# Performance work log

Hardware: AMD Instinct MI355X
Metric: run time of the kernel (lower is better)

The kernel has to match this reference:

```python
import jax, jax.numpy as jnp
import numpy as np

D_MODEL = 1024
N_HEADS = 16
FEAT_DIM = 16   # q/k head dim before feature-map expansion
V_DIM = 64      # v head dim = d_model / n_heads
EPS = 1e-12


def taylor_exp(x):
    """2nd-order Taylor approx feature map of exp(q^T k / sqrt(d)).
    x: (b, h, l, d) -> (b, h, l, 1 + d + d^2)
    f(x) = [1, x / d^{1/4}, vec(x x^T) / (sqrt(2) * sqrt(d))]
    """
    d = x.shape[-1]
    rd = jnp.sqrt(jnp.float32(d))          # sqrt(d)
    rrd = jnp.sqrt(rd)                     # d^{1/4}
    r2 = jnp.sqrt(jnp.float32(2.0))
    x2 = (x[..., :, None] * x[..., None, :]).reshape(*x.shape[:-1], d * d) / r2
    ones = jnp.ones(x.shape[:-1] + (1,), dtype=x.dtype)
    return jnp.concatenate([ones, x / rrd, x2 / rd], axis=-1)


def setup_inputs() -> dict:
    key = jax.random.key(0)
    k0, k1, k2, k3, k4 = jax.random.split(key, 5)
    b, l = 2, 2048
    scale = 1.0 / np.sqrt(D_MODEL)
    return {
        "hidden_states": jax.random.normal(k0, (b, l, D_MODEL), dtype=jnp.float32),
        "Wq": jax.random.normal(k1, (D_MODEL, N_HEADS * FEAT_DIM), dtype=jnp.float32) * scale,
        "Wk": jax.random.normal(k2, (D_MODEL, N_HEADS * FEAT_DIM), dtype=jnp.float32) * scale,
        "Wv": jax.random.normal(k3, (D_MODEL, N_HEADS * V_DIM), dtype=jnp.float32) * scale,
        "Wo": jax.random.normal(k4, (N_HEADS * V_DIM, D_MODEL), dtype=jnp.float32) * scale,
    }


def reference(hidden_states, Wq, Wk, Wv, Wo):
    b, l, _ = hidden_states.shape
    # projections -> (b, h, l, d)
    q = (hidden_states @ Wq).reshape(b, l, N_HEADS, FEAT_DIM).transpose(0, 2, 1, 3)
    k = (hidden_states @ Wk).reshape(b, l, N_HEADS, FEAT_DIM).transpose(0, 2, 1, 3)
    v = (hidden_states @ Wv).reshape(b, l, N_HEADS, V_DIM).transpose(0, 2, 1, 3)

    qf = taylor_exp(q)  # (b, h, l, 273)
    kf = taylor_exp(k)

    # causal linear attention (naive parallel form used by the torch module)
    A = jnp.einsum('bhnf,bhmf->bhnm', qf, kf)
    A = jnp.tril(A)
    y = jnp.einsum('bhnm,bhme->bhne', A, v)
    # denominator: q_f . cumsum(k_f)
    z = 1.0 / (jnp.einsum('bhlf,bhlf->bhl', qf, jnp.cumsum(kf, axis=2)) + EPS)
    y = y * z[..., None]

    out = y.transpose(0, 2, 1, 3).reshape(b, l, N_HEADS * V_DIM) @ Wo
    return out
```

## Files before the change

### kernel.cpp

```cpp
#include <hip/hip_runtime.h>
#include <hip/hip_bf16.h>

#define BATCH 2
#define LSEQ 2048
#define DMODEL 1024
#define NH 16
#define DQK 16
#define DV 64
#define FDIM 273
#define CHUNK 128
#define NCH (LSEQ / CHUNK)
#define ROWS (BATCH * LSEQ)
#define NBH (BATCH * NH)
#define NBC (NBH * NCH)
#define QKVW 1536
#define C2 0.17677669529663687f

typedef short bf16x8 __attribute__((ext_vector_type(8)));
typedef float f32x4 __attribute__((ext_vector_type(4)));

__device__ __forceinline__ unsigned short f2bf(float f) {
  __hip_bfloat16 h = __float2bfloat16(f);
  unsigned short u; __builtin_memcpy(&u, &h, 2); return u;
}
__device__ __forceinline__ float bf2f(unsigned short u) {
  unsigned int v = (unsigned int)u << 16; float f; __builtin_memcpy(&f, &v, 4); return f;
}

__device__ __forceinline__ void storeC(float* C, size_t off, float v) { C[off] = v; }
__device__ __forceinline__ void storeC(unsigned short* C, size_t off, float v) {
  C[off] = f2bf(v);
}

__global__ __launch_bounds__(256) void prep(
    const float* __restrict__ hs,
    const float* __restrict__ Wq, const float* __restrict__ Wk,
    const float* __restrict__ Wv, const float* __restrict__ Wo,
    unsigned short* __restrict__ hsb,
    unsigned short* __restrict__ wqt, unsigned short* __restrict__ wkt,
    unsigned short* __restrict__ wvt, unsigned short* __restrict__ wot) {
  __shared__ float t[32][33];
  if (blockIdx.z == 4) {
    int bid = blockIdx.y * 32 + blockIdx.x;
    const float4* in4 = (const float4*)hs;
#pragma unroll
    for (int k = 0; k < 4; k++) {
      int i = bid * 1024 + k * 256 + threadIdx.x;
      float4 v = in4[i];
      ushort4 o = {f2bf(v.x), f2bf(v.y), f2bf(v.z), f2bf(v.w)};
      ((ushort4*)hsb)[i] = o;
    }
    return;
  }
  const float* W; unsigned short* Wt; int N;
  switch (blockIdx.z) {
    case 0: W = Wq; Wt = wqt; N = 256; break;
    case 1: W = Wk; Wt = wkt; N = 256; break;
    case 2: W = Wv; Wt = wvt; N = 1024; break;
    default: W = Wo; Wt = wot; N = 1024; break;
  }
  const int nb = blockIdx.x * 32;
  if (nb >= N) return;
  const int kb = blockIdx.y * 32;
  const int tx = threadIdx.x & 31, ty4 = (threadIdx.x >> 5) * 4;
#pragma unroll
  for (int r = 0; r < 4; r++)
    t[ty4 + r][tx] = W[(size_t)(kb + ty4 + r) * N + nb + tx];
  __syncthreads();
#pragma unroll
  for (int r = 0; r < 4; r++)
    Wt[(size_t)(nb + ty4 + r) * DMODEL + kb + tx] = f2bf(t[tx][ty4 + r]);
}

template <typename CT>
__global__ __launch_bounds__(256) void gemm_pipe(
    const unsigned short* __restrict__ A, const unsigned short* __restrict__ Bt,
    CT* __restrict__ C, int M, int N, int K) {
  __shared__ unsigned short Sbuf[4 * 8192];
  const int tid = threadIdx.x;
  const int nwg = gridDim.x * gridDim.y;
  const int bid0 = blockIdx.y * gridDim.x + blockIdx.x;
  const int bid = (bid0 & 7) * (nwg >> 3) + (bid0 >> 3);
  const int bm = (bid / gridDim.x) * 128, bn = (bid % gridDim.x) * 128;
  const int lane = tid & 63;
  const int w = tid >> 6;
  const int qr = (w >> 1) * 64, qc = (w & 1) * 64;
  const int nk = K >> 5;
  f32x4 acc[4][4] = {};

  const unsigned short* gbase[4];
  int loff[4];
#pragma unroll
  for (int j = 0; j < 4; ++j) {
    int c = j * 256 + tid;
    int isB = c >> 9;
    int cc = c & 511;
    int row = ((cc >> 6) << 4) + (cc & 15);
    int kh = (cc >> 4) & 3;
    gbase[j] = (isB ? Bt + (size_t)(bn + row) * K : A + (size_t)(bm + row) * K) + kh * 8;
    loff[j] = isB * 4096 + cc * 8;
  }
  auto stage = [&](int t) {
    unsigned short* Sb = Sbuf + (size_t)(t & 3) * 8192;
#pragma unroll
    for (int j = 0; j < 4; ++j)
      __builtin_amdgcn_global_load_lds(
          (const __attribute__((address_space(1))) unsigned int*)(const void*)(gbase[j] + (t << 5)),
          (__attribute__((address_space(3))) unsigned int*)(Sb + loff[j]), 16, 0, 0);
  };

  stage(0); stage(1); stage(2);

  for (int tt = 0; tt < nk; tt += 2) {
    if (tt + 3 < nk) {
      stage(tt + 3);
      asm volatile("s_waitcnt vmcnt(8)" ::: "memory");
    } else {
      asm volatile("s_waitcnt vmcnt(0)" ::: "memory");
    }
    __builtin_amdgcn_s_barrier();
    asm volatile("" ::: "memory");

    const unsigned short* Ab0 = Sbuf + (size_t)(tt & 3) * 8192;
    const unsigned short* Ab1 = Sbuf + (size_t)((tt + 1) & 3) * 8192;
    bf16x8 a0[4], b0[4], a1[4], b1[4];
#pragma unroll
    for (int i = 0; i < 4; ++i) {
      a0[i] = *(const bf16x8*)(Ab0 + ((qr >> 4) + i) * 512 + lane * 8);
      b0[i] = *(const bf16x8*)(Ab0 + 4096 + ((qc >> 4) + i) * 512 + lane * 8);
      a1[i] = *(const bf16x8*)(Ab1 + ((qr >> 4) + i) * 512 + lane * 8);
      b1[i] = *(const bf16x8*)(Ab1 + 4096 + ((qc >> 4) + i) * 512 + lane * 8);
    }
    __builtin_amdgcn_s_setprio(1);
#pragma unroll
    for (int i = 0; i < 4; ++i)
#pragma unroll
      for (int jj = 0; jj < 4; ++jj)
        acc[i][jj] = __builtin_amdgcn_mfma_f32_16x16x32_bf16(a0[i], b0[jj], acc[i][jj], 0, 0, 0);
#pragma unroll
    for (int i = 0; i < 4; ++i)
#pragma unroll
      for (int jj = 0; jj < 4; ++jj)
        acc[i][jj] = __builtin_amdgcn_mfma_f32_16x16x32_bf16(a1[i], b1[jj], acc[i][jj], 0, 0, 0);
    __builtin_amdgcn_s_setprio(0);

    asm volatile("" ::: "memory");
    __builtin_amdgcn_s_barrier();
    asm volatile("" ::: "memory");
    if (tt + 4 < nk) stage(tt + 4);
  }

  const int cn = lane & 15, r0 = (lane >> 4) * 4;
#pragma unroll
  for (int i = 0; i < 4; ++i)
#pragma unroll
    for (int jj = 0; jj < 4; ++jj) {
      size_t base = (size_t)(bm + qr + i * 16 + r0) * N + bn + qc + jj * 16 + cn;
#pragma unroll
      for (int r = 0; r < 4; ++r) storeC(C, base + (size_t)r * N, acc[i][jj][r]);
    }
}

__device__ __forceinline__ void stage_Vp(const unsigned short* __restrict__ qkvb,
                                         int row0, int h, int tid, short* Vp) {
#pragma unroll
  for (int it = 0; it < 4; it++) {
    int t = it * 256 + tid;
    int j = t >> 3, e0 = (t & 7) * 8;
    bf16x8 v8 = *(const bf16x8*)(qkvb + (size_t)(row0 + j) * QKVW + 512 + h * 64 + e0);
    int jg = j >> 3, jj = j & 7;
#pragma unroll
    for (int u = 0; u < 8; u++) {
      int e = e0 + u;
      Vp[((e >> 4) * 4 + (jg >> 2)) * 512 + ((jg & 3) * 16 + (e & 15)) * 8 + jj] =
          v8[u];
    }
  }
  {
    int n = tid & 15, jgrp = tid >> 4;
    bf16x8 v8;
#pragma unroll
    for (int u = 0; u < 8; u++) v8[u] = (n == 0) ? (short)0x3F80 : (short)0;
    *(bf16x8*)(Vp + (16 + (jgrp >> 2)) * 512 + ((jgrp & 3) * 16 + n) * 8) = v8;
  }
}

__global__ __launch_bounds__(256) void chunk_sums_mfma(
    const unsigned short* __restrict__ qkvb, unsigned short* __restrict__ Sfrag) {
  const int c = blockIdx.x, bh = blockIdx.y;
  const int b = bh >> 4, h = bh & 15;
  const int tid = threadIdx.x;
  const int lane = tid & 63, w = tid >> 6;
  const int row0 = b * LSEQ + c * CHUNK;

  __shared__ float ksT[16 * 132];
  __shared__ short SH[56 * 512];
  short* Vp = SH;
  short* Kf0 = SH + 20 * 512;
  short* Kf1 = SH + 38 * 512;

  {
    int i = tid >> 1, d0 = (tid & 1) * 8;
    bf16x8 k8 = *(const bf16x8*)(qkvb + (size_t)(row0 + i) * QKVW + 256 + h * 16 + d0);
#pragma unroll
    for (int j = 0; j < 8; j++) ksT[(d0 + j) * 132 + i] = bf2f((unsigned short)k8[j]);
  }
  stage_Vp(qkvb, row0, h, tid, Vp);
  __syncthreads();

  auto gen = [&](int kt, short* dst) {
    for (int o = tid; o < 1152; o += 256) {
      int mt = o >> 6, w6 = o & 63;
      int kh = w6 >> 4, m = w6 & 15;
      int f = mt * 16 + m;
      int i0 = kt * 32 + kh * 8;
      bf16x8 v8;
      if (f == 0) {
#pragma unroll
        for (int j = 0; j < 8; j++) v8[j] = (short)0x3F80;
      } else if (f < 17) {
        const float* ka = &ksT[(f - 1) * 132 + i0];
        float4 a0 = *(const float4*)ka, a1 = *(const float4*)(ka + 4);
        v8[0] = (short)f2bf(0.5f * a0.x); v8[1] = (short)f2bf(0.5f * a0.y);
        v8[2] = (short)f2bf(0.5f * a0.z); v8[3] = (short)f2bf(0.5f * a0.w);
        v8[4] = (short)f2bf(0.5f * a1.x); v8[5] = (short)f2bf(0.5f * a1.y);
        v8[6] = (short)f2bf(0.5f * a1.z); v8[7] = (short)f2bf(0.5f * a1.w);
      } else if (f < FDIM) {
        int ix = f - 17;
        const float* ka = &ksT[(ix >> 4) * 132 + i0];
        const float* kb2 = &ksT[(ix & 15) * 132 + i0];
        float4 a0 = *(const float4*)ka, a1 = *(const float4*)(ka + 4);
        float4 b0 = *(const float4*)kb2, b1 = *(const float4*)(kb2 + 4);
        v8[0] = (short)f2bf(C2 * a0.x * b0.x); v8[1] = (short)f2bf(C2 * a0.y * b0.y);
        v8[2] = (short)f2bf(C2 * a0.z * b0.z); v8[3] = (short)f2bf(C2 * a0.w * b0.w);
        v8[4] = (short)f2bf(C2 * a1.x * b1.x); v8[5] = (short)f2bf(C2 * a1.y * b1.y);
        v8[6] = (short)f2bf(C2 * a1.z * b1.z); v8[7] = (short)f2bf(C2 * a1.w * b1.w);
      } else {
#pragma unroll
        for (int j = 0; j < 8; j++) v8[j] = 0;
      }
      *(bf16x8*)(dst + mt * 512 + (kh * 16 + m) * 8) = v8;
    }
  };

  gen(0, Kf0);
  __syncthreads();

  f32x4 acc[5][5] = {};
  const int nmt = (w < 2) ? 5 : 4;
  for (int kt = 0; kt < 4; kt++) {
    short* cur = (kt & 1) ? Kf1 : Kf0;
    if (kt < 3) gen(kt + 1, (kt & 1) ? Kf0 : Kf1);
    bf16x8 bv[5];
#pragma unroll
    for (int nt = 0; nt < 5; nt++)
      bv[nt] = *(const bf16x8*)(Vp + (nt * 4 + kt) * 512 + lane * 8);
#pragma unroll
    for (int t2 = 0; t2 < 5; t2++) {
      if (t2 < nmt) {
        int mt = w + t2 * 4;
        bf16x8 av = *(const bf16x8*)(cur + mt * 512 + lane * 8);
#pragma unroll
        for (int nt = 0; nt < 5; nt++)
          acc[t2][nt] = __builtin_amdgcn_mfma_f32_16x16x32_bf16(av, bv[nt], acc[t2][nt], 0, 0, 0);
      }
    }
    __syncthreads();
  }

  const int cl = lane & 15, r0q = (lane >> 4) * 4;
#pragma unroll
  for (int t2 = 0; t2 < 5; t2++) {
    if (t2 < nmt) {
      int mt = w + t2 * 4;
#pragma unroll
      for (int reg = 0; reg < 4; reg++) {
        int f = mt * 16 + r0q + reg;
#pragma unroll
        for (int nt = 0; nt < 5; nt++) {
          int e = nt * 16 + cl;
          SH[((f >> 5) * 5 + nt) * 512 + (((f >> 3) & 3) * 16 + (e & 15)) * 8 + (f & 7)] =
              (short)f2bf(acc[t2][nt][reg]);
        }
      }
    }
  }
  __syncthreads();
  unsigned short* dst = Sfrag + ((size_t)bh * NCH + c) * 45 * 512;
  for (int o = tid; o < 2880; o += 256)
    *(bf16x8*)(dst + o * 8) = *(const bf16x8*)(SH + o * 8);
}

__global__ __launch_bounds__(64) void prefix_scan_frag(
    const unsigned short* __restrict__ Sfrag, unsigned short* __restrict__ PG) {
  const int kt5 = blockIdx.x, bh = blockIdx.y;
  const int lane = threadIdx.x;
  float run[8] = {0.f, 0.f, 0.f, 0.f, 0.f, 0.f, 0.f, 0.f};
  const size_t base = ((size_t)bh * NCH * 45 + kt5) * 512 + lane * 8;
#pragma unroll
  for (int cc = 0; cc < NCH; cc++) {
    size_t a = base + (size_t)cc * 45 * 512;
    bf16x8 s8 = *(const bf16x8*)(Sfrag + a);
    bf16x8 o8;
#pragma unroll
    for (int j = 0; j < 8; j++) {
      o8[j] = (short)f2bf(run[j]);
      run[j] += bf2f((unsigned short)s8[j]);
    }
    *(bf16x8*)(PG + a) = o8;
  }
}

__global__ __launch_bounds__(256) void attn_mfma(
    const unsigned short* __restrict__ qkvb, const unsigned short* __restrict__ PG,
    unsigned short* __restrict__ ybuf) {
  const int c = blockIdx.x, bh = blockIdx.y;
  const int b = bh >> 4, h = bh & 15;
  const int tid = threadIdx.x;
  const int lane = tid & 63, w = tid >> 6;
  const int row0 = b * LSEQ + c * CHUNK;

  __shared__ short U[36864];
  __shared__ float denL[128];
  unsigned short* Uu = (unsigned short*)U;

  const int qrow = (w >> 1) * 64 + lane;
  const int shalf = w & 1;
  bf16x8 qa = *(const bf16x8*)(qkvb + (size_t)(row0 + qrow) * QKVW + h * 16);
  bf16x8 qb = *(const bf16x8*)(qkvb + (size_t)(row0 + qrow) * QKVW + h * 16 + 8);

  for (int t = tid; t < 1024; t += 256) {
    int isK = t >> 9;
    int tt = t & 511;
    int i = tt >> 2, kh = tt & 3;
    bf16x8 v8 = {0, 0, 0, 0, 0, 0, 0, 0};
    if (kh < 2)
      v8 = *(const bf16x8*)(qkvb + (size_t)(row0 + i) * QKVW + isK * 256 + h * 16 + kh * 8);
    *(bf16x8*)(U + isK * 4096 + (i >> 4) * 512 + (kh * 16 + (i & 15)) * 8) = v8;
  }
  __syncthreads();

  {
    bf16x8 aq[2];
#pragma unroll
    for (int mi = 0; mi < 2; mi++)
      aq[mi] = *(const bf16x8*)(U + (w * 2 + mi) * 512 + lane * 8);
    f32x4 S[2][8] = {};
#pragma unroll
    for (int nt = 0; nt < 8; nt++) {
      bf16x8 bk = *(const bf16x8*)(U + 4096 + nt * 512 + lane * 8);
#pragma unroll
      for (int mi = 0; mi < 2; mi++)
        S[mi][nt] = __builtin_amdgcn_mfma_f32_16x16x32_bf16(aq[mi], bk, S[mi][nt], 0, 0, 0);
    }
    const int cl = lane & 15, r0q = (lane >> 4) * 4;
#pragma unroll
    for (int mi = 0; mi < 2; mi++)
#pragma unroll
      for (int nt = 0; nt < 8; nt++)
#pragma unroll
        for (int reg = 0; reg < 4; reg++) {
          int i = (w * 2 + mi) * 16 + r0q + reg;
          int j = nt * 16 + cl;
          float s = S[mi][nt][reg];
          float aij = (j <= i) ? fmaf(s, fmaf(s, 0.03125f, 0.25f), 1.0f) : 0.0f;
          U[8192 + ((i >> 4) * 4 + (j >> 5)) * 512 +
            (((j >> 3) & 3) * 16 + (i & 15)) * 8 + (j & 7)] = (short)f2bf(aij);
        }
  }
  stage_Vp(qkvb, row0, h, tid, U + 24576);
  __syncthreads();

  f32x4 Y[2][5] = {};
#pragma unroll
  for (int kc = 0; kc < 4; kc++) {
    bf16x8 a2[2];
#pragma unroll
    for (int mi = 0; mi < 2; mi++)
      a2[mi] = *(const bf16x8*)(U + 8192 + ((w * 2 + mi) * 4 + kc) * 512 + lane * 8);
#pragma unroll
    for (int nt = 0; nt < 5; nt++) {
      bf16x8 b2 = *(const bf16x8*)(U + 24576 + (nt * 4 + kc) * 512 + lane * 8);
#pragma unroll
      for (int mi = 0; mi < 2; mi++)
        Y[mi][nt] = __builtin_amdgcn_mfma_f32_16x16x32_bf16(a2[mi], b2, Y[mi][nt], 0, 0, 0);
    }
  }
  __syncthreads();

  {
    float qv[16], cq[16];
#pragma unroll
    for (int j = 0; j < 8; j++) {
      qv[j] = bf2f((unsigned short)qa[j]);
      qv[8 + j] = bf2f((unsigned short)qb[j]);
    }
#pragma unroll
    for (int j = 0; j < 16; j++) cq[j] = C2 * qv[j];
    unsigned short* qbase = Uu + (qrow >> 4) * 512 + (qrow & 15) * 8;
    if (shalf == 0) {
#pragma unroll
      for (int vk = 0; vk < 18; vk++) {
        bf16x8 v8;
#pragma unroll
        for (int j = 0; j < 8; j++) {
          int f = vk * 8 + j;
          float qf;
          if (f == 0) qf = 1.0f;
          else if (f < 17) qf = 0.5f * qv[f - 1];
          else { int ix = f - 17; qf = cq[ix >> 4] * qv[ix & 15]; }
          v8[j] = (short)f2bf(qf);
        }
        *(bf16x8*)(qbase + (vk >> 2) * 4096 + (vk & 3) * 128) = v8;
      }
    } else {
#pragma unroll
      for (int vk = 18; vk < 36; vk++) {
        bf16x8 v8;
#pragma unroll
        for (int j = 0; j < 8; j++) {
          int f = vk * 8 + j;
          float qf;
          if (f < FDIM) { int ix = f - 17; qf = cq[ix >> 4] * qv[ix & 15]; }
          else qf = 0.0f;
          v8[j] = (short)f2bf(qf);
        }
        *(bf16x8*)(qbase + (vk >> 2) * 4096 + (vk & 3) * 128) = v8;
      }
    }
  }
  __syncthreads();

  const unsigned short* pgl = PG + ((size_t)bh * NCH + c) * 45 * 512 + lane * 8;
#pragma unroll
  for (int ft = 0; ft < 9; ft++) {
    bf16x8 b3[5];
#pragma unroll
    for (int nt = 0; nt < 5; nt++)
      b3[nt] = *(const bf16x8*)(pgl + (ft * 5 + nt) * 512);
    bf16x8 a3[2];
#pragma unroll
    for (int mi = 0; mi < 2; mi++)
      a3[mi] = *(const bf16x8*)(U + ft * 4096 + (w * 2 + mi) * 512 + lane * 8);
#pragma unroll
    for (int nt = 0; nt < 5; nt++)
#pragma unroll
      for (int mi = 0; mi < 2; mi++)
        Y[mi][nt] = __builtin_amdgcn_mfma_f32_16x16x32_bf16(a3[mi], b3[nt], Y[mi][nt], 0, 0, 0);
  }

  const int cl = lane & 15, r0q = (lane >> 4) * 4;
  if (cl == 0) {
#pragma unroll
    for (int mi = 0; mi < 2; mi++)
#pragma unroll
      for (int reg = 0; reg < 4; reg++)
        denL[(w * 2 + mi) * 16 + r0q + reg] = Y[mi][4][reg];
  }
  __syncthreads();
#pragma unroll
  for (int mi = 0; mi < 2; mi++) {
    float invd[4];
#pragma unroll
    for (int reg = 0; reg < 4; reg++)
      invd[reg] = 1.0f / (denL[(w * 2 + mi) * 16 + r0q + reg] + 1e-12f);
#pragma unroll
    for (int nt = 0; nt < 4; nt++)
#pragma unroll
      for (int reg = 0; reg < 4; reg++) {
        int i = (w * 2 + mi) * 16 + r0q + reg;
        int e = nt * 16 + cl;
        ybuf[(size_t)(row0 + i) * (NH * DV) + h * DV + e] =
            f2bf(Y[mi][nt][reg] * invd[reg]);
      }
  }
}

extern "C" void kernel_launch(void* const* d_in, const int* in_sizes, int n_in,
                              void* d_out, int out_size, void* d_ws, size_t ws_size,
                              hipStream_t stream) {
  const float* hs = (const float*)d_in[0];
  const float* Wq = (const float*)d_in[1];
  const float* Wk = (const float*)d_in[2];
  const float* Wv = (const float*)d_in[3];
  const float* Wo = (const float*)d_in[4];
  float* out = (float*)d_out;

  unsigned short* qkvb  = (unsigned short*)d_ws;
  unsigned short* Sfrag = qkvb + (size_t)ROWS * QKVW;
  unsigned short* PG    = Sfrag + (size_t)NBC * 45 * 512;
  unsigned short* hsb   = PG + (size_t)NBC * 45 * 512;
  unsigned short* yb    = hsb;
  unsigned short* wqt   = hsb + (size_t)ROWS * DMODEL;
  unsigned short* wkt   = wqt + (size_t)(NH * DQK) * DMODEL;
  unsigned short* wvt   = wkt + (size_t)(NH * DQK) * DMODEL;
  unsigned short* wot   = wvt + (size_t)(NH * DV) * DMODEL;

  prep<<<dim3(32, 32, 5), 256, 0, stream>>>(hs, Wq, Wk, Wv, Wo, hsb, wqt, wkt, wvt, wot);

  gemm_pipe<unsigned short><<<dim3(QKVW / 128, ROWS / 128), 256, 0, stream>>>(
      hsb, wqt, qkvb, ROWS, QKVW, DMODEL);

  chunk_sums_mfma<<<dim3(NCH, NBH), 256, 0, stream>>>(qkvb, Sfrag);
  prefix_scan_frag<<<dim3(45, NBH), 64, 0, stream>>>(Sfrag, PG);
  attn_mfma<<<dim3(NCH, NBH), 256, 0, stream>>>(qkvb, PG, yb);

  gemm_pipe<float><<<dim3(DMODEL / 128, ROWS / 128), 256, 0, stream>>>(
      yb, wot, out, ROWS, DMODEL, DMODEL);
}
```

Before: 167.8 us.

## Use 512-thread GEMM blocks and split-K with atomics for output projection

The GEMM kernel now runs 8 waves per block, each computing a 32x64 sub-tile instead of 64x64, which halves per-wave accumulators and global-to-LDS loads per thread. The output projection is split along K into two halves whose partial sums are combined with float atomicAdd into an output zeroed by an extra prep slice. This targets the low block count of the 1024-wide output GEMM (256 tiles) by doubling the number of blocks. The cost is extra atomic traffic and a zeroing pass over the output, plus nondeterministic float summation order. The vmcnt wait counts are adjusted for the smaller per-thread load count.

Result: slower. 191.0 us (+13.8%).

```diff
diff --git a/kernel.cpp b/kernel.cpp
--- a/kernel.cpp
+++ b/kernel.cpp
@@ -38,8 +38,18 @@
     const float* __restrict__ Wv, const float* __restrict__ Wo,
     unsigned short* __restrict__ hsb,
     unsigned short* __restrict__ wqt, unsigned short* __restrict__ wkt,
-    unsigned short* __restrict__ wvt, unsigned short* __restrict__ wot) {
+    unsigned short* __restrict__ wvt, unsigned short* __restrict__ wot,
+    float* __restrict__ out) {
   __shared__ float t[32][33];
+  if (blockIdx.z == 5) {
+    int bid = blockIdx.y * 32 + blockIdx.x;
+    float4 z = {0.f, 0.f, 0.f, 0.f};
+    float4* o4 = (float4*)out;
+#pragma unroll
+    for (int k = 0; k < 4; k++)
+      o4[bid * 1024 + k * 256 + threadIdx.x] = z;
+    return;
+  }
   if (blockIdx.z == 4) {
     int bid = blockIdx.y * 32 + blockIdx.x;
     const float4* in4 = (const float4*)hs;
@@ -72,8 +82,8 @@
     Wt[(size_t)(nb + ty4 + r) * DMODEL + kb + tx] = f2bf(t[tx][ty4 + r]);
 }
 
-template <typename CT>
-__global__ __launch_bounds__(256) void gemm_pipe(
+template <typename CT, int SPLITK>
+__global__ __launch_bounds__(512) void gemm_pipe(
     const unsigned short* __restrict__ A, const unsigned short* __restrict__ Bt,
     CT* __restrict__ C, int M, int N, int K) {
   __shared__ unsigned short Sbuf[4 * 8192];
@@ -84,26 +94,29 @@
   const int bm = (bid / gridDim.x) * 128, bn = (bid % gridDim.x) * 128;
   const int lane = tid & 63;
   const int w = tid >> 6;
-  const int qr = (w >> 1) * 64, qc = (w & 1) * 64;
-  const int nk = K >> 5;
-  f32x4 acc[4][4] = {};
-
-  const unsigned short* gbase[4];
-  int loff[4];
-#pragma unroll
-  for (int j = 0; j < 4; ++j) {
-    int c = j * 256 + tid;
+  const int qr = (w >> 1) * 32, qc = (w & 1) * 64;
+  const int KS = K / SPLITK;
+  const int kbase = blockIdx.z * KS;
+  const int nk = KS >> 5;
+  f32x4 acc[2][4] = {};
+
+  const unsigned short* gbase[2];
+  int loff[2];
+#pragma unroll
+  for (int j = 0; j < 2; ++j) {
+    int c = j * 512 + tid;
     int isB = c >> 9;
     int cc = c & 511;
     int row = ((cc >> 6) << 4) + (cc & 15);
     int kh = (cc >> 4) & 3;
-    gbase[j] = (isB ? Bt + (size_t)(bn + row) * K : A + (size_t)(bm + row) * K) + kh * 8;
+    gbase[j] = (isB ? Bt + (size_t)(bn + row) * K : A + (size_t)(bm + row) * K) +
+               kbase + kh * 8;
     loff[j] = isB * 4096 + cc * 8;
   }
   auto stage = [&](int t) {
     unsigned short* Sb = Sbuf + (size_t)(t & 3) * 8192;
 #pragma unroll
-    for (int j = 0; j < 4; ++j)
+    for (int j = 0; j < 2; ++j)
       __builtin_amdgcn_global_load_lds(
           (const __attribute__((address_space(1))) unsigned int*)(const void*)(gbase[j] + (t << 5)),
           (__attribute__((address_space(3))) unsigned int*)(Sb + loff[j]), 16, 0, 0);
@@ -114,7 +127,9 @@
   for (int tt = 0; tt < nk; tt += 2) {
     if (tt + 3 < nk) {
       stage(tt + 3);
-      asm volatile("s_waitcnt vmcnt(8)" ::: "memory");
+      asm volatile("s_waitcnt vmcnt(4)" ::: "memory");
+    } else if (tt + 3 == nk) {
+      asm volatile("s_waitcnt vmcnt(2)" ::: "memory");
     } else {
       asm volatile("s_waitcnt vmcnt(0)" ::: "memory");
     }
@@ -123,22 +138,25 @@
 
     const unsigned short* Ab0 = Sbuf + (size_t)(tt & 3) * 8192;
     const unsigned short* Ab1 = Sbuf + (size_t)((tt + 1) & 3) * 8192;
-    bf16x8 a0[4], b0[4], a1[4], b1[4];
+    bf16x8 a0[2], b0[4], a1[2], b1[4];
+#pragma unroll
+    for (int i = 0; i < 2; ++i) {
+      a0[i] = *(const bf16x8*)(Ab0 + ((qr >> 4) + i) * 512 + lane * 8);
+      a1[i] = *(const bf16x8*)(Ab1 + ((qr >> 4) + i) * 512 + lane * 8);
+    }
 #pragma unroll
     for (int i = 0; i < 4; ++i) {
-      a0[i] = *(const bf16x8*)(Ab0 + ((qr >> 4) + i) * 512 + lane * 8);
       b0[i] = *(const bf16x8*)(Ab0 + 4096 + ((qc >> 4) + i) * 512 + lane * 8);
-      a1[i] = *(const bf16x8*)(Ab1 + ((qr >> 4) + i) * 512 + lane * 8);
       b1[i] = *(const bf16x8*)(Ab1 + 4096 + ((qc >> 4) + i) * 512 + lane * 8);
     }
     __builtin_amdgcn_s_setprio(1);
 #pragma unroll
-    for (int i = 0; i < 4; ++i)
+    for (int i = 0; i < 2; ++i)
 #pragma unroll
       for (int jj = 0; jj < 4; ++jj)
         acc[i][jj] = __builtin_amdgcn_mfma_f32_16x16x32_bf16(a0[i], b0[jj], acc[i][jj], 0, 0, 0);
 #pragma unroll
-    for (int i = 0; i < 4; ++i)
+    for (int i = 0; i < 2; ++i)
 #pragma unroll
       for (int jj = 0; jj < 4; ++jj)
         acc[i][jj] = __builtin_amdgcn_mfma_f32_16x16x32_bf16(a1[i], b1[jj], acc[i][jj], 0, 0, 0);
@@ -152,12 +170,18 @@
 
   const int cn = lane & 15, r0 = (lane >> 4) * 4;
 #pragma unroll
-  for (int i = 0; i < 4; ++i)
+  for (int i = 0; i < 2; ++i)
 #pragma unroll
     for (int jj = 0; jj < 4; ++jj) {
       size_t base = (size_t)(bm + qr + i * 16 + r0) * N + bn + qc + jj * 16 + cn;
 #pragma unroll
-      for (int r = 0; r < 4; ++r) storeC(C, base + (size_t)r * N, acc[i][jj][r]);
+      for (int r = 0; r < 4; ++r) {
+        if constexpr (SPLITK == 1) {
+          storeC(C, base + (size_t)r * N, acc[i][jj][r]);
+        } else {
+          atomicAdd((float*)&C[base + (size_t)r * N], acc[i][jj][r]);
+        }
+      }
     }
 }
 
@@ -496,15 +520,16 @@
   unsigned short* wvt   = wkt + (size_t)(NH * DQK) * DMODEL;
   unsigned short* wot   = wvt + (size_t)(NH * DV) * DMODEL;
 
-  prep<<<dim3(32, 32, 5), 256, 0, stream>>>(hs, Wq, Wk, Wv, Wo, hsb, wqt, wkt, wvt, wot);
-
-  gemm_pipe<unsigned short><<<dim3(QKVW / 128, ROWS / 128), 256, 0, stream>>>(
+  prep<<<dim3(32, 32, 6), 256, 0, stream>>>(hs, Wq, Wk, Wv, Wo, hsb, wqt, wkt,
+                                            wvt, wot, out);
+
+  gemm_pipe<unsigned short, 1><<<dim3(QKVW / 128, ROWS / 128, 1), 512, 0, stream>>>(
       hsb, wqt, qkvb, ROWS, QKVW, DMODEL);
 
   chunk_sums_mfma<<<dim3(NCH, NBH), 256, 0, stream>>>(qkvb, Sfrag);
   prefix_scan_frag<<<dim3(45, NBH), 64, 0, stream>>>(Sfrag, PG);
   attn_mfma<<<dim3(NCH, NBH), 256, 0, stream>>>(qkvb, PG, yb);
 
-  gemm_pipe<float><<<dim3(DMODEL / 128, ROWS / 128), 256, 0, stream>>>(
+  gemm_pipe<float, 2><<<dim3(DMODEL / 128, ROWS / 128, 2), 512, 0, stream>>>(
       yb, wot, out, ROWS, DMODEL, DMODEL);
 }
```

## Switch GEMM to double-buffered LDS pipeline with higher occupancy

Applied to the files above, without the earlier changes.

Replaces the 4-stage LDS ring, which processed two K-tiles per iteration with prefetch depth 3, with a 2-buffer scheme that issues one K-tile prefetch per iteration. LDS use is halved and launch bounds request 3 blocks per CU, so latency is hidden through occupancy rather than a deep prefetch. The trade-off is a full vmcnt(0) wait and a barrier every K step, which exposes more load latency per workgroup.

Result: slower. 175.8 us (+4.8%).

```diff
diff --git a/kernel.cpp b/kernel.cpp
--- a/kernel.cpp
+++ b/kernel.cpp
@@ -73,10 +73,10 @@
 }
 
 template <typename CT>
-__global__ __launch_bounds__(256) void gemm_pipe(
+__global__ __launch_bounds__(256, 3) void gemm_pipe(
     const unsigned short* __restrict__ A, const unsigned short* __restrict__ Bt,
     CT* __restrict__ C, int M, int N, int K) {
-  __shared__ unsigned short Sbuf[4 * 8192];
+  __shared__ unsigned short Sbuf[2 * 8192];
   const int tid = threadIdx.x;
   const int nwg = gridDim.x * gridDim.y;
   const int bid0 = blockIdx.y * gridDim.x + blockIdx.x;
@@ -101,7 +101,7 @@
     loff[j] = isB * 4096 + cc * 8;
   }
   auto stage = [&](int t) {
-    unsigned short* Sb = Sbuf + (size_t)(t & 3) * 8192;
+    unsigned short* Sb = Sbuf + (size_t)(t & 1) * 8192;
 #pragma unroll
     for (int j = 0; j < 4; ++j)
       __builtin_amdgcn_global_load_lds(
@@ -109,45 +109,34 @@
           (__attribute__((address_space(3))) unsigned int*)(Sb + loff[j]), 16, 0, 0);
   };
 
-  stage(0); stage(1); stage(2);
-
-  for (int tt = 0; tt < nk; tt += 2) {
-    if (tt + 3 < nk) {
-      stage(tt + 3);
-      asm volatile("s_waitcnt vmcnt(8)" ::: "memory");
-    } else {
+  stage(0);
+  asm volatile("s_waitcnt vmcnt(0)" ::: "memory");
+  __builtin_amdgcn_s_barrier();
+  asm volatile("" ::: "memory");
+
+  for (int t = 0; t < nk; ++t) {
+    if (t + 1 < nk) stage(t + 1);
+
+    const unsigned short* Ab = Sbuf + (size_t)(t & 1) * 8192;
+    bf16x8 a[4], b[4];
+#pragma unroll
+    for (int i = 0; i < 4; ++i) {
+      a[i] = *(const bf16x8*)(Ab + ((qr >> 4) + i) * 512 + lane * 8);
+      b[i] = *(const bf16x8*)(Ab + 4096 + ((qc >> 4) + i) * 512 + lane * 8);
+    }
+    __builtin_amdgcn_s_setprio(1);
+#pragma unroll
+    for (int i = 0; i < 4; ++i)
+#pragma unroll
+      for (int jj = 0; jj < 4; ++jj)
+        acc[i][jj] = __builtin_amdgcn_mfma_f32_16x16x32_bf16(a[i], b[jj], acc[i][jj], 0, 0, 0);
+    __builtin_amdgcn_s_setprio(0);
+
+    if (t + 1 < nk) {
       asm volatile("s_waitcnt vmcnt(0)" ::: "memory");
-    }
-    __builtin_amdgcn_s_barrier();
-    asm volatile("" ::: "memory");
-
-    const unsigned short* Ab0 = Sbuf + (size_t)(tt & 3) * 8192;
-    const unsigned short* Ab1 = Sbuf + (size_t)((tt + 1) & 3) * 8192;
-    bf16x8 a0[4], b0[4], a1[4], b1[4];
-#pragma unroll
-    for (int i = 0; i < 4; ++i) {
-      a0[i] = *(const bf16x8*)(Ab0 + ((qr >> 4) + i) * 512 + lane * 8);
-      b0[i] = *(const bf16x8*)(Ab0 + 4096 + ((qc >> 4) + i) * 512 + lane * 8);
-      a1[i] = *(const bf16x8*)(Ab1 + ((qr >> 4) + i) * 512 + lane * 8);
-      b1[i] = *(const bf16x8*)(Ab1 + 4096 + ((qc >> 4) + i) * 512 + lane * 8);
-    }
-    __builtin_amdgcn_s_setprio(1);
-#pragma unroll
-    for (int i = 0; i < 4; ++i)
-#pragma unroll
-      for (int jj = 0; jj < 4; ++jj)
-        acc[i][jj] = __builtin_amdgcn_mfma_f32_16x16x32_bf16(a0[i], b0[jj], acc[i][jj], 0, 0, 0);
-#pragma unroll
-    for (int i = 0; i < 4; ++i)
-#pragma unroll
-      for (int jj = 0; jj < 4; ++jj)
-        acc[i][jj] = __builtin_amdgcn_mfma_f32_16x16x32_bf16(a1[i], b1[jj], acc[i][jj], 0, 0, 0);
-    __builtin_amdgcn_s_setprio(0);
-
-    asm volatile("" ::: "memory");
-    __builtin_amdgcn_s_barrier();
-    asm volatile("" ::: "memory");
-    if (tt + 4 < nk) stage(tt + 4);
+      __builtin_amdgcn_s_barrier();
+      asm volatile("" ::: "memory");
+    }
   }
 
   const int cn = lane & 15, r0 = (lane >> 4) * 4;
```

## Shrink attn_mfma LDS footprint by splitting Q-feature staging into two phases

Applied to the files above, without the earlier changes.

Shared memory for attn_mfma is cut from about 72KB to about 52KB. V is staged into the start of the buffer, which the Q/K staging no longer needs, and the A tile is moved. The expanded Q feature tile is built and consumed in two halves (feature tiles 0-4, then 5-8) so only five tiles are resident at once. Launch bounds request 3 blocks per CU to raise occupancy, at the cost of extra barriers, duplicated q-feature setup, and possible register pressure.

New measurement: 168.0 us. Within noise of the previous version (+0.1%).

```diff
diff --git a/kernel.cpp b/kernel.cpp
--- a/kernel.cpp
+++ b/kernel.cpp
@@ -311,7 +311,7 @@
   }
 }
 
-__global__ __launch_bounds__(256) void attn_mfma(
+__global__ __launch_bounds__(256, 3) void attn_mfma(
     const unsigned short* __restrict__ qkvb, const unsigned short* __restrict__ PG,
     unsigned short* __restrict__ ybuf) {
   const int c = blockIdx.x, bh = blockIdx.y;
@@ -320,7 +320,7 @@
   const int lane = tid & 63, w = tid >> 6;
   const int row0 = b * LSEQ + c * CHUNK;
 
-  __shared__ short U[36864];
+  __shared__ short U[26624];
   __shared__ float denL[128];
   unsigned short* Uu = (unsigned short*)U;
 
@@ -364,11 +364,12 @@
           int j = nt * 16 + cl;
           float s = S[mi][nt][reg];
           float aij = (j <= i) ? fmaf(s, fmaf(s, 0.03125f, 0.25f), 1.0f) : 0.0f;
-          U[8192 + ((i >> 4) * 4 + (j >> 5)) * 512 +
+          U[10240 + ((i >> 4) * 4 + (j >> 5)) * 512 +
             (((j >> 3) & 3) * 16 + (i & 15)) * 8 + (j & 7)] = (short)f2bf(aij);
         }
   }
-  stage_Vp(qkvb, row0, h, tid, U + 24576);
+  __syncthreads();
+  stage_Vp(qkvb, row0, h, tid, U);
   __syncthreads();
 
   f32x4 Y[2][5] = {};
@@ -377,16 +378,35 @@
     bf16x8 a2[2];
 #pragma unroll
     for (int mi = 0; mi < 2; mi++)
-      a2[mi] = *(const bf16x8*)(U + 8192 + ((w * 2 + mi) * 4 + kc) * 512 + lane * 8);
+      a2[mi] = *(const bf16x8*)(U + 10240 + ((w * 2 + mi) * 4 + kc) * 512 + lane * 8);
 #pragma unroll
     for (int nt = 0; nt < 5; nt++) {
-      bf16x8 b2 = *(const bf16x8*)(U + 24576 + (nt * 4 + kc) * 512 + lane * 8);
+      bf16x8 b2 = *(const bf16x8*)(U + (nt * 4 + kc) * 512 + lane * 8);
 #pragma unroll
       for (int mi = 0; mi < 2; mi++)
         Y[mi][nt] = __builtin_amdgcn_mfma_f32_16x16x32_bf16(a2[mi], b2, Y[mi][nt], 0, 0, 0);
     }
   }
   __syncthreads();
+
+  unsigned short* qbase = Uu + (qrow >> 4) * 512 + (qrow & 15) * 8;
+  const unsigned short* pgl = PG + ((size_t)bh * NCH + c) * 45 * 512 + lane * 8;
+
+#define GEN_VK(vk, ftl, qv, cq)                                         \
+  {                                                                     \
+    bf16x8 v8;                                                          \
+    _Pragma("unroll")                                                   \
+    for (int j = 0; j < 8; j++) {                                       \
+      int f = (vk) * 8 + j;                                             \
+      float qf;                                                         \
+      if (f == 0) qf = 1.0f;                                            \
+      else if (f < 17) qf = 0.5f * qv[f - 1];                           \
+      else if (f < FDIM) { int ix = f - 17; qf = cq[ix >> 4] * qv[ix & 15]; } \
+      else qf = 0.0f;                                                   \
+      v8[j] = (short)f2bf(qf);                                          \
+    }                                                                   \
+    *(bf16x8*)(qbase + (ftl) * 4096 + ((vk) & 3) * 128) = v8;           \
+  }
 
   {
     float qv[16], cq[16];
@@ -397,43 +417,18 @@
     }
 #pragma unroll
     for (int j = 0; j < 16; j++) cq[j] = C2 * qv[j];
-    unsigned short* qbase = Uu + (qrow >> 4) * 512 + (qrow & 15) * 8;
     if (shalf == 0) {
 #pragma unroll
-      for (int vk = 0; vk < 18; vk++) {
-        bf16x8 v8;
-#pragma unroll
-        for (int j = 0; j < 8; j++) {
-          int f = vk * 8 + j;
-          float qf;
-          if (f == 0) qf = 1.0f;
-          else if (f < 17) qf = 0.5f * qv[f - 1];
-          else { int ix = f - 17; qf = cq[ix >> 4] * qv[ix & 15]; }
-          v8[j] = (short)f2bf(qf);
-        }
-        *(bf16x8*)(qbase + (vk >> 2) * 4096 + (vk & 3) * 128) = v8;
-      }
+      for (int vk = 0; vk < 10; vk++) GEN_VK(vk, vk >> 2, qv, cq);
     } else {
 #pragma unroll
-      for (int vk = 18; vk < 36; vk++) {
-        bf16x8 v8;
-#pragma unroll
-        for (int j = 0; j < 8; j++) {
-          int f = vk * 8 + j;
-          float qf;
-          if (f < FDIM) { int ix = f - 17; qf = cq[ix >> 4] * qv[ix & 15]; }
-          else qf = 0.0f;
-          v8[j] = (short)f2bf(qf);
-        }
-        *(bf16x8*)(qbase + (vk >> 2) * 4096 + (vk & 3) * 128) = v8;
-      }
-    }
-  }
-  __syncthreads();
-
-  const unsigned short* pgl = PG + ((size_t)bh * NCH + c) * 45 * 512 + lane * 8;
-#pragma unroll
-  for (int ft = 0; ft < 9; ft++) {
+      for (int vk = 10; vk < 20; vk++) GEN_VK(vk, vk >> 2, qv, cq);
+    }
+  }
+  __syncthreads();
+
+#pragma unroll
+  for (int ft = 0; ft < 5; ft++) {
     bf16x8 b3[5];
 #pragma unroll
     for (int nt = 0; nt < 5; nt++)
@@ -448,6 +443,44 @@
       for (int mi = 0; mi < 2; mi++)
         Y[mi][nt] = __builtin_amdgcn_mfma_f32_16x16x32_bf16(a3[mi], b3[nt], Y[mi][nt], 0, 0, 0);
   }
+  __syncthreads();
+
+  {
+    float qv[16], cq[16];
+#pragma unroll
+    for (int j = 0; j < 8; j++) {
+      qv[j] = bf2f((unsigned short)qa[j]);
+      qv[8 + j] = bf2f((unsigned short)qb[j]);
+    }
+#pragma unroll
+    for (int j = 0; j < 16; j++) cq[j] = C2 * qv[j];
+    if (shalf == 0) {
+#pragma unroll
+      for (int vk = 20; vk < 28; vk++) GEN_VK(vk, (vk >> 2) - 5, qv, cq);
+    } else {
+#pragma unroll
+      for (int vk = 28; vk < 36; vk++) GEN_VK(vk, (vk >> 2) - 5, qv, cq);
+    }
+  }
+  __syncthreads();
+
+#pragma unroll
+  for (int ft = 5; ft < 9; ft++) {
+    bf16x8 b3[5];
+#pragma unroll
+    for (int nt = 0; nt < 5; nt++)
+      b3[nt] = *(const bf16x8*)(pgl + (ft * 5 + nt) * 512);
+    bf16x8 a3[2];
+#pragma unroll
+    for (int mi = 0; mi < 2; mi++)
+      a3[mi] = *(const bf16x8*)(U + (ft - 5) * 4096 + (w * 2 + mi) * 512 + lane * 8);
+#pragma unroll
+    for (int nt = 0; nt < 5; nt++)
+#pragma unroll
+      for (int mi = 0; mi < 2; mi++)
+        Y[mi][nt] = __builtin_amdgcn_mfma_f32_16x16x32_bf16(a3[mi], b3[nt], Y[mi][nt], 0, 0, 0);
+  }
+#undef GEN_VK
 
   const int cl = lane & 15, r0q = (lane >> 4) * 4;
   if (cl == 0) {
```
